# Performance work log

Measured on AMD Instinct MI355X. Metric: run time of the kernel, lower is better.

Reference implementation:

```python
import jax, jax.numpy as jnp
import numpy as np

N_HEAD = 12
N_EMBED = 768

def setup_inputs() -> dict:
    key = jax.random.key(0)
    ks = jax.random.split(key, 5)
    B, T, C = 8, 1024, N_EMBED
    s_in = 1.0 / np.sqrt(C)
    s3 = 1.0 / np.sqrt(3 * C)
    return {
        "x": jax.random.normal(ks[0], (B, T, C), dtype=jnp.float32),
        "W_qkv": jax.random.normal(ks[1], (C, 3 * C), dtype=jnp.float32) * s_in,
        "b_qkv": jnp.zeros((3 * C,), dtype=jnp.float32),
        "W_out": jax.random.normal(ks[2], (C, C), dtype=jnp.float32) * s_in,
        "b_out": jnp.zeros((C,), dtype=jnp.float32),
    }

def reference(x, W_qkv, b_qkv, W_out, b_out):
    B, T, C = x.shape
    H = N_HEAD
    d_k = C // H
    qkv = x @ W_qkv + b_qkv  # [B,T,3C]
    q, k, v = jnp.split(qkv, 3, axis=-1)
    # [B,H,T,d]
    q = q.reshape(B, T, H, d_k).transpose(0, 2, 1, 3)
    k = k.reshape(B, T, H, d_k).transpose(0, 2, 1, 3)
    v = v.reshape(B, T, H, d_k).transpose(0, 2, 1, 3)
    logits = jnp.einsum('bhqd,bhkd->bhqk', q, k) * (d_k ** -0.5)
    causal = jnp.tril(jnp.ones((T, T), dtype=bool))
    logits = jnp.where(causal, logits, -jnp.inf)
    scores = jax.nn.softmax(logits, axis=-1)
    out = jnp.einsum('bhqk,bhkd->bhqd', scores, v)
    out = out.transpose(0, 2, 1, 3).reshape(B, T, C)
    return out @ W_out + b_out
```

## Files before the change

kernel.cpp:

```cpp
#include <hip/hip_runtime.h>
#include <stdint.h>

#define B_ 8
#define T_ 1024
#define C_ 768
#define H_ 12
#define DK 64
#define BT (B_*T_)
#define NQKV (3*C_)

typedef unsigned short u16;
typedef __bf16 bf16x8 __attribute__((ext_vector_type(8)));
typedef __bf16 bf16x4 __attribute__((ext_vector_type(4)));
typedef float  f32x4  __attribute__((ext_vector_type(4)));

typedef const __attribute__((address_space(1))) void gvoid_t;
typedef __attribute__((address_space(3))) void lvoid_t;

#define WC_VM8   0xF78
#define WC_VM4   0xF74
#define WC_VM0   0xF70
#define WC_LGKM0 0xC07F

__device__ __forceinline__ void gl_lds16(const void* g, void* l) {
    __builtin_amdgcn_global_load_lds((gvoid_t*)g, (lvoid_t*)l, 16, 0, 0);
}

__device__ __forceinline__ u16 f2b(float f) {
    union { float f; unsigned int u; } v; v.f = f;
    unsigned int u = v.u;
    return (u16)((u + 0x7fffu + ((u >> 16) & 1u)) >> 16);
}

__device__ __forceinline__ f32x4 mfma16(bf16x8 a, bf16x8 b, f32x4 c) {
    return __builtin_amdgcn_mfma_f32_16x16x32_bf16(a, b, c, 0, 0, 0);
}

__global__ void k_convert(const float* __restrict__ in, u16* __restrict__ out, int n4) {
    int i = blockIdx.x * blockDim.x + threadIdx.x;
    if (i < n4) {
        float4 f = ((const float4*)in)[i];
        uint2 o;
        o.x = (unsigned)f2b(f.x) | ((unsigned)f2b(f.y) << 16);
        o.y = (unsigned)f2b(f.z) | ((unsigned)f2b(f.w) << 16);
        ((uint2*)out)[i] = o;
    }
}

__global__ __launch_bounds__(256)
void k_transpose_convert(const float* __restrict__ w, u16* __restrict__ wt,
                         int K, int N) {
    __shared__ u16 tile[32][34];
    const int tx = threadIdx.x, ty = threadIdx.y;
    const int n0 = blockIdx.x * 32, k0 = blockIdx.y * 32;
    #pragma unroll
    for (int i = 0; i < 4; i++)
        tile[ty + i * 8][tx] = f2b(w[(size_t)(k0 + ty + i * 8) * N + n0 + tx]);
    __syncthreads();
    #pragma unroll
    for (int i = 0; i < 4; i++)
        wt[(size_t)(n0 + ty + i * 8) * K + k0 + tx] = tile[tx][ty + i * 8];
}

template <int EPI>
__global__ __launch_bounds__(256, 3)
void k_gemm(const u16* __restrict__ A, const u16* __restrict__ Bt,
            const float* __restrict__ bias,
            u16* __restrict__ qo, u16* __restrict__ ko, u16* __restrict__ vto,
            float* __restrict__ outf, int M, int N, int K)
{
    __shared__ u16 As[3][128 * 32];
    __shared__ u16 Bs[3][128 * 32];
    const int tid  = threadIdx.x;
    const int lane = tid & 63;
    const int w    = tid >> 6;
    const int quad = lane >> 4;
    const int col  = lane & 15;

    const int id   = blockIdx.x + gridDim.x * blockIdx.y;
    const int xcd  = id & 7;
    const int slot = id >> 3;
    const int m0   = (xcd * 8 + (slot & 7)) * 128;
    const int n0   = (slot >> 3) * 128;

    const int wm   = (w >> 1) * 64;
    const int wn   = (w & 1) * 64;

    f32x4 zero4 = {0.f, 0.f, 0.f, 0.f};
    f32x4 acc[4][4];
    #pragma unroll
    for (int i = 0; i < 4; i++)
        #pragma unroll
        for (int j = 0; j < 4; j++) acc[i][j] = zero4;

    const int sr  = tid >> 2;
    const int scc = ((tid & 3) ^ ((sr >> 1) & 3)) * 8;
    const u16* gA = A  + (size_t)(m0 + sr) * K + scc;
    const u16* gB = Bt + (size_t)(n0 + sr) * K + scc;

    const int NIT = K >> 5;

    #define STAGE(kt, bufi)                                                          \
        do {                                                                         \
            gl_lds16(gA + (kt),                  (char*)As[bufi] + w * 1024);        \
            gl_lds16(gA + (size_t)64 * K + (kt), (char*)As[bufi] + 4096 + w * 1024); \
            gl_lds16(gB + (kt),                  (char*)Bs[bufi] + w * 1024);        \
            gl_lds16(gB + (size_t)64 * K + (kt), (char*)Bs[bufi] + 4096 + w * 1024); \
        } while (0)

    STAGE(0, 0);
    if (NIT > 1) STAGE(32, 1);
    int cur = 0;
    for (int it = 0; it < NIT; ++it) {
        __builtin_amdgcn_s_barrier();
        if (it + 2 < NIT) {
            int b2 = cur + 2; if (b2 >= 3) b2 -= 3;
            STAGE((it + 2) << 5, b2);
            __builtin_amdgcn_s_waitcnt(WC_VM8);
        } else if (it + 1 < NIT) {
            __builtin_amdgcn_s_waitcnt(WC_VM4);
        } else {
            __builtin_amdgcn_s_waitcnt(WC_VM0);
        }
        __builtin_amdgcn_s_barrier();

        const u16* Ab = As[cur];
        const u16* Bb = Bs[cur];
        bf16x8 af[4], bfr[4];
        #pragma unroll
        for (int mt = 0; mt < 4; mt++) {
            int row = wm + mt * 16 + col;
            af[mt] = *(const bf16x8*)&Ab[row * 32 + ((quad ^ ((row >> 1) & 3)) * 8)];
        }
        #pragma unroll
        for (int nt = 0; nt < 4; nt++) {
            int row = wn + nt * 16 + col;
            bfr[nt] = *(const bf16x8*)&Bb[row * 32 + ((quad ^ ((row >> 1) & 3)) * 8)];
        }
        #pragma unroll
        for (int mt = 0; mt < 4; mt++)
            #pragma unroll
            for (int nt = 0; nt < 4; nt++)
                acc[mt][nt] = mfma16(af[mt], bfr[nt], acc[mt][nt]);

        cur = (cur == 2) ? 0 : cur + 1;
    }
    #undef STAGE

    #pragma unroll
    for (int mt = 0; mt < 4; mt++) {
        #pragma unroll
        for (int nt = 0; nt < 4; nt++) {
            #pragma unroll
            for (int r = 0; r < 4; r++) {
                int m = m0 + wm + mt * 16 + quad * 4 + r;
                int n = n0 + wn + nt * 16 + col;
                float v = acc[mt][nt][r] + bias[n];
                if constexpr (EPI == 0) {
                    int sec = n / C_;
                    int c   = n - sec * C_;
                    int h   = c >> 6;
                    int d   = c & 63;
                    int b   = m >> 10;
                    int t   = m & 1023;
                    int bh  = b * H_ + h;
                    u16 bv  = f2b(v);
                    if (sec == 0)      qo [((size_t)bh * T_ + t) * DK + d] = bv;
                    else if (sec == 1) ko [((size_t)bh * T_ + t) * DK + d] = bv;
                    else               vto[((size_t)bh * DK + d) * T_ + t] = bv;
                } else {
                    outf[(size_t)m * N + n] = v;
                }
            }
        }
    }
}

#define PSTRIDE 72

__device__ __forceinline__ bf16x8 ld_sw(const u16* base, int row, int half,
                                        int quad, int c7) {
    return *(const bf16x8*)(base + row * DK + (((half * 4 + quad) ^ c7) * 8));
}

template <bool MASK>
__device__ __forceinline__ void attn_chunk(
    const u16* Ks, const u16* Vs, __bf16* pbuf,
    const bf16x8 (&qf)[2][2], bf16x8 ones,
    int kv0, int qw, int quad, int col,
    f32x4 (&oacc)[2][4], f32x4 (&lacc)[2])
{
    const int c7 = col & 7;
    f32x4 zero4 = {0.f, 0.f, 0.f, 0.f};
    f32x4 st[2][4];
    #pragma unroll
    for (int g = 0; g < 4; g++) {
        bf16x8 klo = ld_sw(Ks, g * 16 + col, 0, quad, c7);
        bf16x8 khi = ld_sw(Ks, g * 16 + col, 1, quad, c7);
        st[0][g] = mfma16(khi, qf[0][1], mfma16(klo, qf[0][0], zero4));
        st[1][g] = mfma16(khi, qf[1][1], mfma16(klo, qf[1][0], zero4));
    }
    const float scl = 0.18033688f;
    #pragma unroll
    for (int s = 0; s < 2; s++) {
        __bf16* pb = pbuf + s * 16 * PSTRIDE + col * PSTRIDE;
        #pragma unroll
        for (int g = 0; g < 4; g++) {
            bf16x4 pp;
            #pragma unroll
            for (int r = 0; r < 4; r++) {
                float p = __builtin_amdgcn_exp2f(st[s][g][r] * scl - 12.0f);
                if (MASK) {
                    int kv = kv0 + g * 16 + quad * 4 + r;
                    if (kv > qw + s * 16 + col) p = 0.f;
                }
                pp[r] = (__bf16)p;
            }
            *(bf16x4*)(pb + g * 16 + quad * 4) = pp;
        }
    }
    __builtin_amdgcn_s_waitcnt(WC_LGKM0);
    bf16x8 pf[2][2];
    #pragma unroll
    for (int s = 0; s < 2; s++) {
        const __bf16* pb = pbuf + s * 16 * PSTRIDE + col * PSTRIDE;
        pf[s][0] = *(const bf16x8*)(pb + quad * 8);
        pf[s][1] = *(const bf16x8*)(pb + 32 + quad * 8);
        lacc[s] = mfma16(pf[s][1], ones, mfma16(pf[s][0], ones, lacc[s]));
    }
    #pragma unroll
    for (int dt = 0; dt < 4; dt++) {
        bf16x8 vlo = ld_sw(Vs, dt * 16 + col, 0, quad, c7);
        bf16x8 vhi = ld_sw(Vs, dt * 16 + col, 1, quad, c7);
        #pragma unroll
        for (int s = 0; s < 2; s++)
            oacc[s][dt] = mfma16(pf[s][1], vhi, mfma16(pf[s][0], vlo, oacc[s][dt]));
    }
}

__global__ __launch_bounds__(256, 3)
void k_attn(const u16* __restrict__ Q, const u16* __restrict__ Kf,
            const u16* __restrict__ Vt, u16* __restrict__ Of)
{
    __shared__ u16 Ks[2][64 * DK];
    __shared__ u16 Vs[2][64 * DK];
    __shared__ __bf16 Plds[4][32 * PSTRIDE];
    const int bh   = blockIdx.x;
    const int b    = bh / H_;
    const int h    = bh - b * H_;
    const int tid  = threadIdx.x;
    const int lane = tid & 63;
    const int w    = tid >> 6;
    const int quad = lane >> 4;
    const int col  = lane & 15;
    const int ty   = 7 - (int)blockIdx.y;
    const int nch  = 2 * ty + 2;
    const int qw   = ty * 128 + w * 32;
    __bf16* pbuf = Plds[w];

    const u16* Qb = Q  + (size_t)bh * T_ * DK;
    const u16* Kb = Kf + (size_t)bh * T_ * DK;
    const u16* Vb = Vt + (size_t)bh * DK * T_;

    int sG0 = tid, sG1 = 256 + tid;
    int sr0 = sG0 >> 3, sg0 = (sG0 & 7) ^ (sr0 & 7);
    int sr1 = sG1 >> 3, sg1 = (sG1 & 7) ^ (sr1 & 7);

    bf16x8 qf[2][2];
    #pragma unroll
    for (int s = 0; s < 2; s++) {
        const u16* qp = Qb + (size_t)(qw + s * 16 + col) * DK;
        qf[s][0] = *(const bf16x8*)(qp + quad * 8);
        qf[s][1] = *(const bf16x8*)(qp + 32 + quad * 8);
    }

    bf16x8 ones;
    #pragma unroll
    for (int i = 0; i < 8; i++) ((u16*)&ones)[i] = 0x3F80;

    f32x4 zero4 = {0.f, 0.f, 0.f, 0.f};
    f32x4 oacc[2][4];
    f32x4 lacc[2] = {zero4, zero4};
    #pragma unroll
    for (int s = 0; s < 2; s++)
        #pragma unroll
        for (int dt = 0; dt < 4; dt++) oacc[s][dt] = zero4;

    #define ASTAGE(c, bufi)                                                            \
        do {                                                                           \
            int kvs = (c) * 64;                                                        \
            gl_lds16(Kb + (size_t)(kvs + sr0) * DK + sg0 * 8, (char*)Ks[bufi] + w * 1024);        \
            gl_lds16(Kb + (size_t)(kvs + sr1) * DK + sg1 * 8, (char*)Ks[bufi] + 4096 + w * 1024); \
            gl_lds16(Vb + (size_t)sr0 * T_ + kvs + sg0 * 8,   (char*)Vs[bufi] + w * 1024);        \
            gl_lds16(Vb + (size_t)sr1 * T_ + kvs + sg1 * 8,   (char*)Vs[bufi] + 4096 + w * 1024); \
        } while (0)

    ASTAGE(0, 0);
    #pragma unroll 1
    for (int c = 0; c < nch; ++c) {
        const int cur = c & 1;
        __builtin_amdgcn_s_barrier();
        if (c + 1 < nch) {
            ASTAGE(c + 1, cur ^ 1);
            __builtin_amdgcn_s_waitcnt(WC_VM4);
        } else {
            __builtin_amdgcn_s_waitcnt(WC_VM0);
        }
        __builtin_amdgcn_s_barrier();

        const int kv0 = c * 64;
        if (kv0 <= qw + 31) {
            if (kv0 + 63 <= qw)
                attn_chunk<false>(Ks[cur], Vs[cur], pbuf, qf, ones, kv0, qw, quad, col, oacc, lacc);
            else
                attn_chunk<true>(Ks[cur], Vs[cur], pbuf, qf, ones, kv0, qw, quad, col, oacc, lacc);
        }
    }
    #undef ASTAGE

    #pragma unroll
    for (int s = 0; s < 2; s++) {
        #pragma unroll
        for (int r = 0; r < 4; r++) {
            float inv = 1.f / lacc[s][r];
            int t = qw + s * 16 + quad * 4 + r;
            u16* op = Of + ((size_t)(b * T_ + t)) * C_ + h * DK;
            #pragma unroll
            for (int dt = 0; dt < 4; dt++) op[dt * 16 + col] = f2b(oacc[s][dt][r] * inv);
        }
    }
}

extern "C" void kernel_launch(void* const* d_in, const int* in_sizes, int n_in,
                              void* d_out, int out_size, void* d_ws, size_t ws_size,
                              hipStream_t stream) {
    const float* x    = (const float*)d_in[0];
    const float* Wqkv = (const float*)d_in[1];
    const float* bqkv = (const float*)d_in[2];
    const float* Wout = (const float*)d_in[3];
    const float* bout = (const float*)d_in[4];
    float* out = (float*)d_out;

    char* ws = (char*)d_ws;
    u16* xb    = (u16*)(ws);
    u16* wqkvT = (u16*)(ws + 12582912);
    u16* woutT = (u16*)(ws + 16121856);
    u16* qw    = (u16*)(ws + 17301504);
    u16* kw    = (u16*)(ws + 29884416);
    u16* vtw   = (u16*)(ws + 42467328);
    u16* aw    = (u16*)(ws + 55050240);

    k_convert<<<(BT * C_ / 4) / 256, 256, 0, stream>>>(x, xb, BT * C_ / 4);
    k_transpose_convert<<<dim3(NQKV / 32, C_ / 32), dim3(32, 8), 0, stream>>>(Wqkv, wqkvT, C_, NQKV);
    k_transpose_convert<<<dim3(C_ / 32, C_ / 32), dim3(32, 8), 0, stream>>>(Wout, woutT, C_, C_);

    k_gemm<0><<<dim3(NQKV / 128, BT / 128), 256, 0, stream>>>(
        xb, wqkvT, bqkv, qw, kw, vtw, nullptr, BT, NQKV, C_);

    k_attn<<<dim3(B_ * H_, 8), 256, 0, stream>>>(qw, kw, vtw, aw);

    k_gemm<1><<<dim3(C_ / 128, BT / 128), 256, 0, stream>>>(
        aw, woutT, bout, nullptr, nullptr, nullptr, out, BT, C_, C_);
}
```

Baseline: 190.1 us.

## Use 256x128 tiles for QKV GEMM and switch waits to inline asm

Splits the templated GEMM into a dedicated QKV kernel with a 256x128 block tile. Each wave now computes a 64x128 sub-tile with a 4x8 MFMA accumulator array, which raises data reuse per LDS load and halves the grid to 576 blocks, with occupancy lowered to 2 blocks per CU. Barriers and waitcnts are now emitted as inline asm instead of builtins, which changes how the compiler can schedule around them. The output GEMM is specialized to a float epilogue. The larger tile uses more registers and LDS, and the smaller grid may not fill all CUs evenly.

New measurement: 196.5 us. 3.4% more time.

```diff
diff --git a/kernel.cpp b/kernel.cpp
--- a/kernel.cpp
+++ b/kernel.cpp
@@ -17,10 +17,8 @@
 typedef const __attribute__((address_space(1))) void gvoid_t;
 typedef __attribute__((address_space(3))) void lvoid_t;
 
-#define WC_VM8   0xF78
-#define WC_VM4   0xF74
-#define WC_VM0   0xF70
-#define WC_LGKM0 0xC07F
+#define SBARRIER()  asm volatile("s_barrier" ::: "memory")
+#define SWAITCNT(s) asm volatile("s_waitcnt " s ::: "memory")
 
 __device__ __forceinline__ void gl_lds16(const void* g, void* l) {
     __builtin_amdgcn_global_load_lds((gvoid_t*)g, (lvoid_t*)l, 16, 0, 0);
@@ -62,12 +60,119 @@
         wt[(size_t)(n0 + ty + i * 8) * K + k0 + tx] = tile[tx][ty + i * 8];
 }
 
-template <int EPI>
+__global__ __launch_bounds__(256, 2)
+void k_gemm_qkv(const u16* __restrict__ A, const u16* __restrict__ Bt,
+                const float* __restrict__ bias,
+                u16* __restrict__ qo, u16* __restrict__ ko, u16* __restrict__ vto)
+{
+    const int K = C_;
+    __shared__ u16 As[3][256 * 32];
+    __shared__ u16 Bs[3][128 * 32];
+    const int tid  = threadIdx.x;
+    const int lane = tid & 63;
+    const int w    = tid >> 6;
+    const int quad = lane >> 4;
+    const int col  = lane & 15;
+
+    const int id   = blockIdx.x;
+    const int xcd  = id & 7;
+    const int slot = id >> 3;
+    const int m0   = (xcd * 4 + (slot & 3)) * 256;
+    const int n0   = (slot >> 2) * 128;
+
+    f32x4 zero4 = {0.f, 0.f, 0.f, 0.f};
+    f32x4 acc[4][8];
+    #pragma unroll
+    for (int i = 0; i < 4; i++)
+        #pragma unroll
+        for (int j = 0; j < 8; j++) acc[i][j] = zero4;
+
+    const int srl = lane >> 2;
+    const int scc = ((lane & 3) ^ ((lane >> 3) & 3)) * 8;
+    const u16* gA = A  + (size_t)(m0 + w * 16 + srl) * K + scc;
+    const u16* gB = Bt + (size_t)(n0 + w * 16 + srl) * K + scc;
+
+    const int NIT = K >> 5;
+
+    #define STAGE(kt, bufi)                                                            \
+        do {                                                                           \
+            gl_lds16(gA + (kt),                   (char*)As[bufi] + w * 1024);         \
+            gl_lds16(gA + (size_t)64  * K + (kt), (char*)As[bufi] + 4096  + w * 1024); \
+            gl_lds16(gA + (size_t)128 * K + (kt), (char*)As[bufi] + 8192  + w * 1024); \
+            gl_lds16(gA + (size_t)192 * K + (kt), (char*)As[bufi] + 12288 + w * 1024); \
+            gl_lds16(gB + (kt),                   (char*)Bs[bufi] + w * 1024);         \
+            gl_lds16(gB + (size_t)64  * K + (kt), (char*)Bs[bufi] + 4096  + w * 1024); \
+        } while (0)
+
+    STAGE(0, 0);
+    STAGE(32, 1);
+    int cur = 0;
+    const int sw = ((col >> 1) & 3);
+    for (int it = 0; it < NIT; ++it) {
+        SBARRIER();
+        if (it + 2 < NIT) {
+            int b2 = cur + 2; if (b2 >= 3) b2 -= 3;
+            STAGE((it + 2) << 5, b2);
+            SWAITCNT("vmcnt(12)");
+        } else if (it + 1 < NIT) {
+            SWAITCNT("vmcnt(6)");
+        } else {
+            SWAITCNT("vmcnt(0)");
+        }
+        SBARRIER();
+
+        const u16* Ab = As[cur];
+        const u16* Bb = Bs[cur];
+        bf16x8 af[4], bfr[8];
+        #pragma unroll
+        for (int mt = 0; mt < 4; mt++) {
+            int row = w * 64 + mt * 16 + col;
+            af[mt] = *(const bf16x8*)&Ab[row * 32 + ((quad ^ sw) * 8)];
+        }
+        #pragma unroll
+        for (int nt = 0; nt < 8; nt++) {
+            int row = nt * 16 + col;
+            bfr[nt] = *(const bf16x8*)&Bb[row * 32 + ((quad ^ sw) * 8)];
+        }
+        #pragma unroll
+        for (int mt = 0; mt < 4; mt++)
+            #pragma unroll
+            for (int nt = 0; nt < 8; nt++)
+                acc[mt][nt] = mfma16(af[mt], bfr[nt], acc[mt][nt]);
+
+        cur = (cur == 2) ? 0 : cur + 1;
+    }
+    #undef STAGE
+
+    #pragma unroll
+    for (int mt = 0; mt < 4; mt++) {
+        #pragma unroll
+        for (int nt = 0; nt < 8; nt++) {
+            #pragma unroll
+            for (int r = 0; r < 4; r++) {
+                int m = m0 + w * 64 + mt * 16 + quad * 4 + r;
+                int n = n0 + nt * 16 + col;
+                float v = acc[mt][nt][r] + bias[n];
+                int sec = n / C_;
+                int c   = n - sec * C_;
+                int h   = c >> 6;
+                int d   = c & 63;
+                int b   = m >> 10;
+                int t   = m & 1023;
+                int bh  = b * H_ + h;
+                u16 bv  = f2b(v);
+                if (sec == 0)      qo [((size_t)bh * T_ + t) * DK + d] = bv;
+                else if (sec == 1) ko [((size_t)bh * T_ + t) * DK + d] = bv;
+                else               vto[((size_t)bh * DK + d) * T_ + t] = bv;
+            }
+        }
+    }
+}
+
 __global__ __launch_bounds__(256, 3)
-void k_gemm(const u16* __restrict__ A, const u16* __restrict__ Bt,
-            const float* __restrict__ bias,
-            u16* __restrict__ qo, u16* __restrict__ ko, u16* __restrict__ vto,
-            float* __restrict__ outf, int M, int N, int K)
+void k_gemm_out(const u16* __restrict__ A, const u16* __restrict__ Bt,
+                const float* __restrict__ bias, float* __restrict__ outf,
+                int M, int N, int K)
 {
     __shared__ u16 As[3][128 * 32];
     __shared__ u16 Bs[3][128 * 32];
@@ -109,20 +214,20 @@
         } while (0)
 
     STAGE(0, 0);
-    if (NIT > 1) STAGE(32, 1);
+    STAGE(32, 1);
     int cur = 0;
     for (int it = 0; it < NIT; ++it) {
-        __builtin_amdgcn_s_barrier();
+        SBARRIER();
         if (it + 2 < NIT) {
             int b2 = cur + 2; if (b2 >= 3) b2 -= 3;
             STAGE((it + 2) << 5, b2);
-            __builtin_amdgcn_s_waitcnt(WC_VM8);
+            SWAITCNT("vmcnt(8)");
         } else if (it + 1 < NIT) {
-            __builtin_amdgcn_s_waitcnt(WC_VM4);
+            SWAITCNT("vmcnt(4)");
         } else {
-            __builtin_amdgcn_s_waitcnt(WC_VM0);
-        }
-        __builtin_amdgcn_s_barrier();
+            SWAITCNT("vmcnt(0)");
+        }
+        SBARRIER();
 
         const u16* Ab = As[cur];
         const u16* Bb = Bs[cur];
@@ -155,22 +260,7 @@
             for (int r = 0; r < 4; r++) {
                 int m = m0 + wm + mt * 16 + quad * 4 + r;
                 int n = n0 + wn + nt * 16 + col;
-                float v = acc[mt][nt][r] + bias[n];
-                if constexpr (EPI == 0) {
-                    int sec = n / C_;
-                    int c   = n - sec * C_;
-                    int h   = c >> 6;
-                    int d   = c & 63;
-                    int b   = m >> 10;
-                    int t   = m & 1023;
-                    int bh  = b * H_ + h;
-                    u16 bv  = f2b(v);
-                    if (sec == 0)      qo [((size_t)bh * T_ + t) * DK + d] = bv;
-                    else if (sec == 1) ko [((size_t)bh * T_ + t) * DK + d] = bv;
-                    else               vto[((size_t)bh * DK + d) * T_ + t] = bv;
-                } else {
-                    outf[(size_t)m * N + n] = v;
-                }
+                outf[(size_t)m * N + n] = acc[mt][nt][r] + bias[n];
             }
         }
     }
@@ -219,7 +309,7 @@
             *(bf16x4*)(pb + g * 16 + quad * 4) = pp;
         }
     }
-    __builtin_amdgcn_s_waitcnt(WC_LGKM0);
+    SWAITCNT("lgkmcnt(0)");
     bf16x8 pf[2][2];
     #pragma unroll
     for (int s = 0; s < 2; s++) {
@@ -299,14 +389,14 @@
     #pragma unroll 1
     for (int c = 0; c < nch; ++c) {
         const int cur = c & 1;
-        __builtin_amdgcn_s_barrier();
+        SBARRIER();
         if (c + 1 < nch) {
             ASTAGE(c + 1, cur ^ 1);
-            __builtin_amdgcn_s_waitcnt(WC_VM4);
+            SWAITCNT("vmcnt(4)");
         } else {
-            __builtin_amdgcn_s_waitcnt(WC_VM0);
-        }
-        __builtin_amdgcn_s_barrier();
+            SWAITCNT("vmcnt(0)");
+        }
+        SBARRIER();
 
         const int kv0 = c * 64;
         if (kv0 <= qw + 31) {
@@ -354,11 +444,10 @@
     k_transpose_convert<<<dim3(NQKV / 32, C_ / 32), dim3(32, 8), 0, stream>>>(Wqkv, wqkvT, C_, NQKV);
     k_transpose_convert<<<dim3(C_ / 32, C_ / 32), dim3(32, 8), 0, stream>>>(Wout, woutT, C_, C_);
 
-    k_gemm<0><<<dim3(NQKV / 128, BT / 128), 256, 0, stream>>>(
-        xb, wqkvT, bqkv, qw, kw, vtw, nullptr, BT, NQKV, C_);
+    k_gemm_qkv<<<576, 256, 0, stream>>>(xb, wqkvT, bqkv, qw, kw, vtw);
 
     k_attn<<<dim3(B_ * H_, 8), 256, 0, stream>>>(qw, kw, vtw, aw);
 
-    k_gemm<1><<<dim3(C_ / 128, BT / 128), 256, 0, stream>>>(
-        aw, woutT, bout, nullptr, nullptr, nullptr, out, BT, C_, C_);
-}
+    k_gemm_out<<<dim3(C_ / 128, BT / 128), 256, 0, stream>>>(
+        aw, woutT, bout, out, BT, C_, C_);
+}
```
